# Kernel tuning notes

Hardware: AMD Instinct MI355X
Metric: run time of the kernel (lower is better)

The kernel has to match this reference:

```python
import jax, jax.numpy as jnp
import numpy as np

KH, KW = 3, 3
STRIDE, PAD, DIL = 1, 1, 1


def setup_inputs() -> dict:
    key = jax.random.key(0)
    k1, k2, k3 = jax.random.split(key, 3)
    B, C, H, W, O = 8, 128, 64, 64, 128
    x = jax.random.normal(k1, (B, C, H, W), jnp.float32)
    # offset layout: [B, 2*K, Ho, Wo], pairs (dy, dx) per kernel tap
    offset = jax.random.normal(k2, (B, 2 * KH * KW, H, W), jnp.float32)
    n = C * KH * KW
    stdv = 1.0 / np.sqrt(n)
    weight = jax.random.uniform(k3, (O, C, KH, KW), jnp.float32, -stdv, stdv)
    bias = jnp.zeros((O,), jnp.float32)
    return {"x": x, "offset": offset, "weight": weight, "bias": bias}


def _deform_conv(x, offset, weight, bias):
    B, C, H, W = x.shape
    O = weight.shape[0]
    K = KH * KW
    Ho = (H + 2 * PAD - DIL * (KH - 1) - 1) // STRIDE + 1
    Wo = (W + 2 * PAD - DIL * (KW - 1) - 1) // STRIDE + 1

    off = offset.reshape(B, K, 2, Ho, Wo)  # (dy, dx) per tap

    # base sampling grid for each kernel tap: [K, Ho, Wo]
    hs = jnp.arange(Ho, dtype=jnp.float32) * STRIDE - PAD
    ws = jnp.arange(Wo, dtype=jnp.float32) * STRIDE - PAD
    ki = jnp.arange(KH, dtype=jnp.float32) * DIL
    kj = jnp.arange(KW, dtype=jnp.float32) * DIL
    base_y = (ki[:, None, None, None] + hs[None, None, :, None])  # [KH,1,Ho,1]
    base_x = (kj[None, :, None, None] + ws[None, None, None, :])  # [1,KW,1,Wo]
    base_y = jnp.broadcast_to(base_y, (KH, KW, Ho, Wo)).reshape(K, Ho, Wo)
    base_x = jnp.broadcast_to(base_x, (KH, KW, Ho, Wo)).reshape(K, Ho, Wo)

    py = base_y[None] + off[:, :, 0]  # [B,K,Ho,Wo]
    px = base_x[None] + off[:, :, 1]

    y0 = jnp.floor(py)
    x0 = jnp.floor(px)
    ly = py - y0  # fractional parts
    lx = px - x0
    y0i = y0.astype(jnp.int32)
    x0i = x0.astype(jnp.int32)

    flat = x.reshape(B, C, H * W)

    def gather(yi, xi, w):
        # zero outside the image (DCN zero-padding semantics)
        valid = (yi >= 0) & (yi < H) & (xi >= 0) & (xi < W)
        idx = jnp.clip(yi, 0, H - 1) * W + jnp.clip(xi, 0, W - 1)  # [B,K,Ho,Wo]
        g = jnp.take_along_axis(flat, idx.reshape(B, 1, -1), axis=2)
        g = g.reshape(B, C, K, Ho, Wo)
        wmask = (w * valid.astype(x.dtype))[:, None]  # [B,1,K,Ho,Wo]
        return g * wmask

    # bilinear accumulation over 4 corners -> im2col columns [B,C,K,Ho,Wo]
    cols = gather(y0i, x0i, (1 - ly) * (1 - lx))
    cols = cols + gather(y0i, x0i + 1, (1 - ly) * lx)
    cols = cols + gather(y0i + 1, x0i, ly * (1 - lx))
    cols = cols + gather(y0i + 1, x0i + 1, ly * lx)

    out = jnp.einsum('ock,bckhw->bohw', weight.reshape(O, C, K), cols)
    return out + bias[None, :, None, None]


def reference(x, offset, weight, bias):
    return _deform_conv(x, offset, weight, bias)
```

## Files before the change

kernel.cpp:

```cpp
#include <hip/hip_runtime.h>


#define BB 8
#define CC 128
#define HH 64
#define WW 64
#define OO 128
#define KTAPS 9

typedef __attribute__((ext_vector_type(8))) short bf16x8;
typedef __attribute__((ext_vector_type(4))) float f32x4;

__device__ __forceinline__ unsigned short f2bf(float f) {
    unsigned u = __float_as_uint(f);
    u += 0x7FFFu + ((u >> 16) & 1u);
    return (unsigned short)(u >> 16);
}
#if __has_builtin(__builtin_amdgcn_cvt_pk_bf16_f32)
typedef __attribute__((ext_vector_type(2))) __bf16 bf16x2_t;
__device__ __forceinline__ unsigned pack2bf(float lo, float hi) {
    bf16x2_t v = __builtin_amdgcn_cvt_pk_bf16_f32(lo, hi);
    unsigned r;
    __builtin_memcpy(&r, &v, 4);
    return r;
}
#else
__device__ __forceinline__ unsigned pack2bf(float lo, float hi) {
    return (unsigned)f2bf(lo) | ((unsigned)f2bf(hi) << 16);
}
#endif
__device__ __forceinline__ float bflo(unsigned p) { return __uint_as_float(p << 16); }
__device__ __forceinline__ float bfhi(unsigned p) { return __uint_as_float(p & 0xFFFF0000u); }

__global__ __launch_bounds__(256)
void prep_kernel(const float* __restrict__ x, const float* __restrict__ wgt,
                 unsigned short* __restrict__ xt, unsigned short* __restrict__ wpk) {
    const int t = threadIdx.x;
    if (blockIdx.x < 512) {
        __shared__ float tile[WW * 132];
        const int b = blockIdx.x >> 6;
        const int h = blockIdx.x & 63;
        const float* src = x + ((size_t)b * CC * HH + h) * WW;
        {
            const int wq = t & 15;
            const int cb = t >> 4;
#pragma unroll
            for (int it = 0; it < 8; ++it) {
                const int c = it * 16 + cb;
                const float4 v = *reinterpret_cast<const float4*>(src + (size_t)c * (HH * WW) + wq * 4);
                tile[(wq * 4 + 0) * 132 + c] = v.x;
                tile[(wq * 4 + 1) * 132 + c] = v.y;
                tile[(wq * 4 + 2) * 132 + c] = v.z;
                tile[(wq * 4 + 3) * 132 + c] = v.w;
            }
        }
        __syncthreads();
        unsigned short* dst = xt + ((size_t)b * HH + h) * WW * CC;
        {
            const int cg = t & 15;
            const int wb = t >> 4;
#pragma unroll
            for (int it = 0; it < 4; ++it) {
                const int w = it * 16 + wb;
                const float* tp = &tile[w * 132 + cg * 8];
                uint4 p;
                p.x = pack2bf(tp[0], tp[1]);
                p.y = pack2bf(tp[2], tp[3]);
                p.z = pack2bf(tp[4], tp[5]);
                p.w = pack2bf(tp[6], tp[7]);
                *reinterpret_cast<uint4*>(&dst[(size_t)w * CC + cg * 8]) = p;
            }
        }
    } else {
        const int id   = (blockIdx.x - 512) * 256 + t;
        const int lane = id & 63;
        const int frag = id >> 6;
        const int nt   = frag & 7;
        const int c0q  = (frag >> 3) & 3;
        const int tap  = frag >> 5;
        const int o    = (nt << 4) + (lane & 15);
        const int c    = (c0q << 5) + ((lane >> 4) << 3);
        const float* s = wgt + ((size_t)o * CC + c) * KTAPS + tap;
        unsigned u[4];
#pragma unroll
        for (int j = 0; j < 4; ++j)
            u[j] = pack2bf(s[(2 * j) * KTAPS], s[(2 * j + 1) * KTAPS]);
        *reinterpret_cast<uint4*>(wpk + (size_t)frag * 512 + lane * 8) =
            make_uint4(u[0], u[1], u[2], u[3]);
    }
}

__global__ __launch_bounds__(256, 2)
void dcn_mfma_kernel(const unsigned short* __restrict__ xt,
                     const unsigned short* __restrict__ wpk,
                     const float* __restrict__ offset,
                     const float* __restrict__ bias,
                     float* __restrict__ out) {
    __shared__ __align__(16) float smem_f[4 * 128 * 20];
    float2* sLL = reinterpret_cast<float2*>(smem_f);
    short2* sYX = reinterpret_cast<short2*>(smem_f + 1152);

    const int t  = threadIdx.x;
    const int b  = blockIdx.x >> 6;
    const int ho = blockIdx.x & 63;

    for (int s = t; s < KTAPS * 64; s += 256) {
        const int k  = s >> 6;
        const int wo = s & 63;
        const int ki = k / 3;
        const int kj = k - ki * 3;
        const float dy = offset[(((size_t)b * 18 + 2 * k    ) * 64 + ho) * 64 + wo];
        const float dx = offset[(((size_t)b * 18 + 2 * k + 1) * 64 + ho) * 64 + wo];
        const float py = (float)(ho - 1 + ki) + dy;
        const float px = (float)(wo - 1 + kj) + dx;
        const float y0f = floorf(py);
        const float x0f = floorf(px);
        sLL[s] = make_float2(py - y0f, px - x0f);
        sYX[s] = make_short2((short)(int)y0f, (short)(int)x0f);
    }
    __syncthreads();

    f32x4 acc[8];
#pragma unroll
    for (int nt = 0; nt < 8; ++nt) acc[nt] = (f32x4){0.f, 0.f, 0.f, 0.f};

    const int lane = t & 63;
    const int wave = t >> 6;
    const int lm   = lane & 15;
    const int quad = lane >> 4;
    const int q16  = quad * 16;
    const int lane16 = lane * 16;
    const char* xb = (const char*)(xt + (size_t)b * HH * WW * CC);
    const char* wb = (const char*)wpk;

    for (int tap = 0; tap < KTAPS; ++tap) {
        const int rec = (tap << 6) + (wave << 4) + lm;
        const float2 ll = sLL[rec];
        const short2 yx = sYX[rec];
        const int y0 = yx.x, x0 = yx.y;
        const int y1 = y0 + 1, x1 = x0 + 1;
        const float ly = ll.x, lx = ll.y;
        const bool vy0 = ((unsigned)y0 < (unsigned)HH);
        const bool vy1 = ((unsigned)y1 < (unsigned)HH);
        const bool vx0 = ((unsigned)x0 < (unsigned)WW);
        const bool vx1 = ((unsigned)x1 < (unsigned)WW);
        const float w00 = (vy0 && vx0) ? (1.f - ly) * (1.f - lx) : 0.f;
        const float w01 = (vy0 && vx1) ? (1.f - ly) * lx         : 0.f;
        const float w10 = (vy1 && vx0) ? ly * (1.f - lx)         : 0.f;
        const float w11 = (vy1 && vx1) ? ly * lx                 : 0.f;
        const int cy0 = min(max(y0, 0), HH - 1);
        const int cy1 = min(max(y1, 0), HH - 1);
        const int cx0 = min(max(x0, 0), WW - 1);
        const int cx1 = min(max(x1, 0), WW - 1);
        const char* base00 = xb + ((((cy0 << 6) + cx0) << 8) + q16);
        const char* base01 = xb + ((((cy0 << 6) + cx1) << 8) + q16);
        const char* base10 = xb + ((((cy1 << 6) + cx0) << 8) + q16);
        const char* base11 = xb + ((((cy1 << 6) + cx1) << 8) + q16);

        uint4 a00 = *reinterpret_cast<const uint4*>(base00);
        uint4 a01 = *reinterpret_cast<const uint4*>(base01);
        uint4 a10 = *reinterpret_cast<const uint4*>(base10);
        uint4 a11 = *reinterpret_cast<const uint4*>(base11);

#pragma unroll
        for (int c0q = 0; c0q < 4; ++c0q) {
            uint4 bfr[8];
            const char* wrow = wb + ((((tap << 5) + (c0q << 3))) << 10) + lane16;
#pragma unroll
            for (int nt = 0; nt < 8; ++nt)
                bfr[nt] = *reinterpret_cast<const uint4*>(wrow + (nt << 10));
            uint4 n00, n01, n10, n11;
            if (c0q < 3) {
                const int cb = (c0q + 1) << 6;
                n00 = *reinterpret_cast<const uint4*>(base00 + cb);
                n01 = *reinterpret_cast<const uint4*>(base01 + cb);
                n10 = *reinterpret_cast<const uint4*>(base10 + cb);
                n11 = *reinterpret_cast<const uint4*>(base11 + cb);
            }
            const unsigned* u00 = reinterpret_cast<const unsigned*>(&a00);
            const unsigned* u01 = reinterpret_cast<const unsigned*>(&a01);
            const unsigned* u10 = reinterpret_cast<const unsigned*>(&a10);
            const unsigned* u11 = reinterpret_cast<const unsigned*>(&a11);
            unsigned afu[4];
#pragma unroll
            for (int j = 0; j < 4; ++j) {
                const float rl = w00 * bflo(u00[j]) + w01 * bflo(u01[j])
                               + w10 * bflo(u10[j]) + w11 * bflo(u11[j]);
                const float rh = w00 * bfhi(u00[j]) + w01 * bfhi(u01[j])
                               + w10 * bfhi(u10[j]) + w11 * bfhi(u11[j]);
                afu[j] = pack2bf(rl, rh);
            }
            bf16x8 afrag;
            __builtin_memcpy(&afrag, afu, 16);
#pragma unroll
            for (int nt = 0; nt < 8; ++nt) {
                bf16x8 bfrag;
                __builtin_memcpy(&bfrag, &bfr[nt], 16);
                acc[nt] = __builtin_amdgcn_mfma_f32_16x16x32_bf16(afrag, bfrag, acc[nt], 0, 0, 0);
            }
            if (c0q < 3) { a00 = n00; a01 = n01; a10 = n10; a11 = n11; }
        }
    }

    __syncthreads();
    float* scr = smem_f + wave * (128 * 20);
#pragma unroll
    for (int nt = 0; nt < 8; ++nt) {
        const int o_l = (nt << 4) + lm;
        *reinterpret_cast<float4*>(&scr[o_l * 20 + (quad << 2)]) =
            make_float4(acc[nt][0], acc[nt][1], acc[nt][2], acc[nt][3]);
    }
#pragma unroll
    for (int h = 0; h < 2; ++h) {
        const int o = (h << 6) + lane;
        const float bv = bias[o];
        float* op = out + (((size_t)(b * OO + o) * HH + ho) << 6) + (wave << 4);
        const float* sr = scr + o * 20;
#pragma unroll
        for (int j = 0; j < 4; ++j) {
            const float4 f = *reinterpret_cast<const float4*>(sr + j * 4);
            *reinterpret_cast<float4*>(op + j * 4) =
                make_float4(f.x + bv, f.y + bv, f.z + bv, f.w + bv);
        }
    }
}

extern "C" void kernel_launch(void* const* d_in, const int* in_sizes, int n_in,
                              void* d_out, int out_size, void* d_ws, size_t ws_size,
                              hipStream_t stream) {
    const float* x      = (const float*)d_in[0];
    const float* offset = (const float*)d_in[1];
    const float* wgt    = (const float*)d_in[2];
    const float* bias   = (const float*)d_in[3];
    float* out = (float*)d_out;

    unsigned short* xt  = (unsigned short*)d_ws;
    unsigned short* wpk = xt + (size_t)BB * HH * WW * CC;

    hipLaunchKernelGGL(prep_kernel, dim3(512 + 72), dim3(256), 0, stream, x, wgt, xt, wpk);
    hipLaunchKernelGGL(dcn_mfma_kernel, dim3(BB * HH), dim3(256), 0, stream,
                       xt, wpk, offset, bias, out);
}
```

Before: 132.6 us.

## Split output row across two blocks and split channel reduction across waves

Each block now handles half an output row (32 pixels). The four waves are arranged as two pixel groups times two channel halves, and the two channel-half partial accumulators are reduced through shared memory. The grid doubles to 1024 blocks and launch bounds rise to 4 blocks per CU, aiming at better occupancy and latency hiding on the gather-heavy loop. The cost is an extra LDS reduction step, and only half the waves do the epilogue.

```diff
diff --git a/kernel.cpp b/kernel.cpp
--- a/kernel.cpp
+++ b/kernel.cpp
@@ -90,25 +90,29 @@
     }
 }
 
-__global__ __launch_bounds__(256, 2)
+__global__ __launch_bounds__(256, 4)
 void dcn_mfma_kernel(const unsigned short* __restrict__ xt,
                      const unsigned short* __restrict__ wpk,
                      const float* __restrict__ offset,
                      const float* __restrict__ bias,
                      float* __restrict__ out) {
-    __shared__ __align__(16) float smem_f[4 * 128 * 20];
-    float2* sLL = reinterpret_cast<float2*>(smem_f);
-    short2* sYX = reinterpret_cast<short2*>(smem_f + 1152);
-
-    const int t  = threadIdx.x;
-    const int b  = blockIdx.x >> 6;
-    const int ho = blockIdx.x & 63;
-
-    for (int s = t; s < KTAPS * 64; s += 256) {
-        const int k  = s >> 6;
-        const int wo = s & 63;
-        const int ki = k / 3;
-        const int kj = k - ki * 3;
+    __shared__ __align__(16) float2 sLL[KTAPS * 32];
+    __shared__ __align__(16) short2 sYX[KTAPS * 32];
+    __shared__ __align__(16) float  dumpf[2 * 2048];
+    __shared__ __align__(16) float  transf[2 * 2560];
+
+    const int t   = threadIdx.x;
+    const int bid = blockIdx.x;
+    const int b   = bid >> 7;
+    const int ho  = (bid >> 1) & 63;
+    const int woh = bid & 1;
+
+    for (int s = t; s < KTAPS * 32; s += 256) {
+        const int k   = s >> 5;
+        const int wol = s & 31;
+        const int wo  = (woh << 5) + wol;
+        const int ki  = k / 3;
+        const int kj  = k - ki * 3;
         const float dy = offset[(((size_t)b * 18 + 2 * k    ) * 64 + ho) * 64 + wo];
         const float dx = offset[(((size_t)b * 18 + 2 * k + 1) * 64 + ho) * 64 + wo];
         const float py = (float)(ho - 1 + ki) + dy;
@@ -126,15 +130,17 @@
 
     const int lane = t & 63;
     const int wave = t >> 6;
+    const int mi   = wave & 1;
+    const int kh   = wave >> 1;
     const int lm   = lane & 15;
     const int quad = lane >> 4;
-    const int q16  = quad * 16;
-    const int lane16 = lane * 16;
     const char* xb = (const char*)(xt + (size_t)b * HH * WW * CC);
     const char* wb = (const char*)wpk;
+    const int cbase  = (kh << 7) + (quad << 4);
+    const int lane16 = lane * 16;
 
     for (int tap = 0; tap < KTAPS; ++tap) {
-        const int rec = (tap << 6) + (wave << 4) + lm;
+        const int rec = (tap << 5) + (mi << 4) + lm;
         const float2 ll = sLL[rec];
         const short2 yx = sYX[rec];
         const int y0 = yx.x, x0 = yx.y;
@@ -152,43 +158,46 @@
         const int cy1 = min(max(y1, 0), HH - 1);
         const int cx0 = min(max(x0, 0), WW - 1);
         const int cx1 = min(max(x1, 0), WW - 1);
-        const char* base00 = xb + ((((cy0 << 6) + cx0) << 8) + q16);
-        const char* base01 = xb + ((((cy0 << 6) + cx1) << 8) + q16);
-        const char* base10 = xb + ((((cy1 << 6) + cx0) << 8) + q16);
-        const char* base11 = xb + ((((cy1 << 6) + cx1) << 8) + q16);
+        const char* base00 = xb + ((((cy0 << 6) + cx0) << 8) + cbase);
+        const char* base01 = xb + ((((cy0 << 6) + cx1) << 8) + cbase);
+        const char* base10 = xb + ((((cy1 << 6) + cx0) << 8) + cbase);
+        const char* base11 = xb + ((((cy1 << 6) + cx1) << 8) + cbase);
 
         uint4 a00 = *reinterpret_cast<const uint4*>(base00);
         uint4 a01 = *reinterpret_cast<const uint4*>(base01);
         uint4 a10 = *reinterpret_cast<const uint4*>(base10);
         uint4 a11 = *reinterpret_cast<const uint4*>(base11);
-
-#pragma unroll
-        for (int c0q = 0; c0q < 4; ++c0q) {
+        uint4 c00 = *reinterpret_cast<const uint4*>(base00 + 64);
+        uint4 c01 = *reinterpret_cast<const uint4*>(base01 + 64);
+        uint4 c10 = *reinterpret_cast<const uint4*>(base10 + 64);
+        uint4 c11 = *reinterpret_cast<const uint4*>(base11 + 64);
+
+        const char* wtap = wb + ((((tap << 2) + (kh << 1)) << 13)) + lane16;
+
+#pragma unroll
+        for (int j = 0; j < 2; ++j) {
             uint4 bfr[8];
-            const char* wrow = wb + ((((tap << 5) + (c0q << 3))) << 10) + lane16;
+            const char* wrow = wtap + (j << 13);
 #pragma unroll
             for (int nt = 0; nt < 8; ++nt)
                 bfr[nt] = *reinterpret_cast<const uint4*>(wrow + (nt << 10));
-            uint4 n00, n01, n10, n11;
-            if (c0q < 3) {
-                const int cb = (c0q + 1) << 6;
-                n00 = *reinterpret_cast<const uint4*>(base00 + cb);
-                n01 = *reinterpret_cast<const uint4*>(base01 + cb);
-                n10 = *reinterpret_cast<const uint4*>(base10 + cb);
-                n11 = *reinterpret_cast<const uint4*>(base11 + cb);
-            }
-            const unsigned* u00 = reinterpret_cast<const unsigned*>(&a00);
-            const unsigned* u01 = reinterpret_cast<const unsigned*>(&a01);
-            const unsigned* u10 = reinterpret_cast<const unsigned*>(&a10);
-            const unsigned* u11 = reinterpret_cast<const unsigned*>(&a11);
+
+            const uint4 va = (j == 0) ? a00 : c00;
+            const uint4 vb = (j == 0) ? a01 : c01;
+            const uint4 vc = (j == 0) ? a10 : c10;
+            const uint4 vd = (j == 0) ? a11 : c11;
+            const unsigned* u00 = reinterpret_cast<const unsigned*>(&va);
+            const unsigned* u01 = reinterpret_cast<const unsigned*>(&vb);
+            const unsigned* u10 = reinterpret_cast<const unsigned*>(&vc);
+            const unsigned* u11 = reinterpret_cast<const unsigned*>(&vd);
             unsigned afu[4];
 #pragma unroll
-            for (int j = 0; j < 4; ++j) {
-                const float rl = w00 * bflo(u00[j]) + w01 * bflo(u01[j])
-                               + w10 * bflo(u10[j]) + w11 * bflo(u11[j]);
-                const float rh = w00 * bfhi(u00[j]) + w01 * bfhi(u01[j])
-                               + w10 * bfhi(u10[j]) + w11 * bfhi(u11[j]);
-                afu[j] = pack2bf(rl, rh);
+            for (int jj = 0; jj < 4; ++jj) {
+                const float rl = w00 * bflo(u00[jj]) + w01 * bflo(u01[jj])
+                               + w10 * bflo(u10[jj]) + w11 * bflo(u11[jj]);
+                const float rh = w00 * bfhi(u00[jj]) + w01 * bfhi(u01[jj])
+                               + w10 * bfhi(u10[jj]) + w11 * bfhi(u11[jj]);
+                afu[jj] = pack2bf(rl, rh);
             }
             bf16x8 afrag;
             __builtin_memcpy(&afrag, afu, 16);
@@ -198,29 +207,43 @@
                 __builtin_memcpy(&bfrag, &bfr[nt], 16);
                 acc[nt] = __builtin_amdgcn_mfma_f32_16x16x32_bf16(afrag, bfrag, acc[nt], 0, 0, 0);
             }
-            if (c0q < 3) { a00 = n00; a01 = n01; a10 = n10; a11 = n11; }
-        }
-    }
-
+        }
+    }
+
+    if (kh == 1) {
+        float* d = dumpf + mi * 2048;
+#pragma unroll
+        for (int nt = 0; nt < 8; ++nt)
+            *reinterpret_cast<float4*>(&d[((nt << 6) + lane) << 2]) =
+                make_float4(acc[nt][0], acc[nt][1], acc[nt][2], acc[nt][3]);
+    }
     __syncthreads();
-    float* scr = smem_f + wave * (128 * 20);
-#pragma unroll
-    for (int nt = 0; nt < 8; ++nt) {
-        const int o_l = (nt << 4) + lm;
-        *reinterpret_cast<float4*>(&scr[o_l * 20 + (quad << 2)]) =
-            make_float4(acc[nt][0], acc[nt][1], acc[nt][2], acc[nt][3]);
-    }
-#pragma unroll
-    for (int h = 0; h < 2; ++h) {
-        const int o = (h << 6) + lane;
-        const float bv = bias[o];
-        float* op = out + (((size_t)(b * OO + o) * HH + ho) << 6) + (wave << 4);
-        const float* sr = scr + o * 20;
-#pragma unroll
-        for (int j = 0; j < 4; ++j) {
-            const float4 f = *reinterpret_cast<const float4*>(sr + j * 4);
-            *reinterpret_cast<float4*>(op + j * 4) =
-                make_float4(f.x + bv, f.y + bv, f.z + bv, f.w + bv);
+    if (kh == 0) {
+        const float* d = dumpf + mi * 2048;
+#pragma unroll
+        for (int nt = 0; nt < 8; ++nt) {
+            const float4 p = *reinterpret_cast<const float4*>(&d[((nt << 6) + lane) << 2]);
+            acc[nt][0] += p.x; acc[nt][1] += p.y; acc[nt][2] += p.z; acc[nt][3] += p.w;
+        }
+        float* scr = transf + mi * 2560;
+#pragma unroll
+        for (int nt = 0; nt < 8; ++nt) {
+            const int o_l = (nt << 4) + lm;
+            *reinterpret_cast<float4*>(&scr[o_l * 20 + (quad << 2)]) =
+                make_float4(acc[nt][0], acc[nt][1], acc[nt][2], acc[nt][3]);
+        }
+#pragma unroll
+        for (int h = 0; h < 2; ++h) {
+            const int o = (h << 6) + lane;
+            const float bv = bias[o];
+            float* op = out + (((size_t)(b * OO + o) * HH + ho) << 6) + (woh << 5) + (mi << 4);
+            const float* sr = scr + o * 20;
+#pragma unroll
+            for (int jj = 0; jj < 4; ++jj) {
+                const float4 f = *reinterpret_cast<const float4*>(sr + jj * 4);
+                *reinterpret_cast<float4*>(op + jj * 4) =
+                    make_float4(f.x + bv, f.y + bv, f.z + bv, f.w + bv);
+            }
         }
     }
 }
@@ -238,6 +261,6 @@
     unsigned short* wpk = xt + (size_t)BB * HH * WW * CC;
 
     hipLaunchKernelGGL(prep_kernel, dim3(512 + 72), dim3(256), 0, stream, x, wgt, xt, wpk);
-    hipLaunchKernelGGL(dcn_mfma_kernel, dim3(BB * HH), dim3(256), 0, stream,
+    hipLaunchKernelGGL(dcn_mfma_kernel, dim3(BB * HH * 2), dim3(256), 0, stream,
                        xt, wpk, offset, bias, out);
 }
```

New measurement: 143.2 us. 1.08x slower.

## Stage per-tap weight fragments in double-buffered LDS via direct global-to-LDS loads

Applied to the files above, without the earlier changes.

Each block now copies the packed bf16 weights for one kernel tap into shared memory with global_load_lds. It double-buffers across taps so the next tap's copy overlaps the current tap's MFMA work. The B fragments are then read from LDS instead of each wave reloading them from global/L2. The block index is remapped so consecutive blocks share the same output row across batches, and the epilogue scratch stride is padded to 21 to reduce bank conflicts. This adds a __syncthreads per tap and a large LDS footprint that may limit occupancy, and float4 accesses at stride 21 are no longer 16-byte aligned.

```diff
diff --git a/kernel.cpp b/kernel.cpp
--- a/kernel.cpp
+++ b/kernel.cpp
@@ -96,17 +96,18 @@
                      const float* __restrict__ offset,
                      const float* __restrict__ bias,
                      float* __restrict__ out) {
-    __shared__ __align__(16) float smem_f[4 * 128 * 20];
-    float2* sLL = reinterpret_cast<float2*>(smem_f);
-    short2* sYX = reinterpret_cast<short2*>(smem_f + 1152);
-
-    const int t  = threadIdx.x;
-    const int b  = blockIdx.x >> 6;
-    const int ho = blockIdx.x & 63;
-
-    for (int s = t; s < KTAPS * 64; s += 256) {
-        const int k  = s >> 6;
-        const int wo = s & 63;
+    __shared__ __align__(16) unsigned short wB[2][16384];
+    __shared__ __align__(16) float2 sLL[KTAPS * 64];
+    __shared__ __align__(16) short2 sYX[KTAPS * 64];
+
+    const int t   = threadIdx.x;
+    const int bid = blockIdx.x;
+    const int b   = bid & 7;
+    const int ho  = bid >> 3;
+
+    for (int r = t; r < KTAPS * 64; r += 256) {
+        const int k  = r >> 6;
+        const int wo = r & 63;
         const int ki = k / 3;
         const int kj = k - ki * 3;
         const float dy = offset[(((size_t)b * 18 + 2 * k    ) * 64 + ho) * 64 + wo];
@@ -115,8 +116,25 @@
         const float px = (float)(wo - 1 + kj) + dx;
         const float y0f = floorf(py);
         const float x0f = floorf(px);
-        sLL[s] = make_float2(py - y0f, px - x0f);
-        sYX[s] = make_short2((short)(int)y0f, (short)(int)x0f);
+        sLL[r] = make_float2(py - y0f, px - x0f);
+        sYX[r] = make_short2((short)(int)y0f, (short)(int)x0f);
+    }
+
+    const char* wb = (const char*)wpk;
+    {
+        const char* wsrc = wb + (t << 4);
+        unsigned short* ldst = &wB[0][t << 3];
+#pragma unroll
+        for (int i = 0; i < 8; ++i) {
+#if __has_builtin(__builtin_amdgcn_global_load_lds)
+            __builtin_amdgcn_global_load_lds(
+                (const __attribute__((address_space(1))) unsigned*)(wsrc + (i << 12)),
+                (__attribute__((address_space(3))) unsigned*)(ldst + (i << 11)), 16, 0, 0);
+#else
+            *reinterpret_cast<uint4*>(ldst + (i << 11)) =
+                *reinterpret_cast<const uint4*>(wsrc + (i << 12));
+#endif
+        }
     }
     __syncthreads();
 
@@ -125,16 +143,31 @@
     for (int nt = 0; nt < 8; ++nt) acc[nt] = (f32x4){0.f, 0.f, 0.f, 0.f};
 
     const int lane = t & 63;
-    const int wave = t >> 6;
+    const int mi   = t >> 6;
     const int lm   = lane & 15;
     const int quad = lane >> 4;
-    const int q16  = quad * 16;
-    const int lane16 = lane * 16;
-    const char* xb = (const char*)(xt + (size_t)b * HH * WW * CC);
-    const char* wb = (const char*)wpk;
-
+    const char* xb = (const char*)xt + ((size_t)b << 20);
+    const int lane8 = lane << 3;
+
+    int curb = 0;
     for (int tap = 0; tap < KTAPS; ++tap) {
-        const int rec = (tap << 6) + (wave << 4) + lm;
+        if (tap < KTAPS - 1) {
+            const char* wsrc = wb + ((tap + 1) << 15) + (t << 4);
+            unsigned short* ldst = &wB[curb ^ 1][t << 3];
+#pragma unroll
+            for (int i = 0; i < 8; ++i) {
+#if __has_builtin(__builtin_amdgcn_global_load_lds)
+                __builtin_amdgcn_global_load_lds(
+                    (const __attribute__((address_space(1))) unsigned*)(wsrc + (i << 12)),
+                    (__attribute__((address_space(3))) unsigned*)(ldst + (i << 11)), 16, 0, 0);
+#else
+                *reinterpret_cast<uint4*>(ldst + (i << 11)) =
+                    *reinterpret_cast<const uint4*>(wsrc + (i << 12));
+#endif
+            }
+        }
+
+        const int rec = (tap << 6) + (mi << 4) + lm;
         const float2 ll = sLL[rec];
         const short2 yx = sYX[rec];
         const int y0 = yx.x, x0 = yx.y;
@@ -152,23 +185,26 @@
         const int cy1 = min(max(y1, 0), HH - 1);
         const int cx0 = min(max(x0, 0), WW - 1);
         const int cx1 = min(max(x1, 0), WW - 1);
-        const char* base00 = xb + ((((cy0 << 6) + cx0) << 8) + q16);
-        const char* base01 = xb + ((((cy0 << 6) + cx1) << 8) + q16);
-        const char* base10 = xb + ((((cy1 << 6) + cx0) << 8) + q16);
-        const char* base11 = xb + ((((cy1 << 6) + cx1) << 8) + q16);
+        const char* base00 = xb + ((((cy0 << 6) + cx0) << 8) + (quad << 4));
+        const char* base01 = xb + ((((cy0 << 6) + cx1) << 8) + (quad << 4));
+        const char* base10 = xb + ((((cy1 << 6) + cx0) << 8) + (quad << 4));
+        const char* base11 = xb + ((((cy1 << 6) + cx1) << 8) + (quad << 4));
 
         uint4 a00 = *reinterpret_cast<const uint4*>(base00);
         uint4 a01 = *reinterpret_cast<const uint4*>(base01);
         uint4 a10 = *reinterpret_cast<const uint4*>(base10);
         uint4 a11 = *reinterpret_cast<const uint4*>(base11);
 
+        const unsigned short* bbuf = wB[curb];
+
 #pragma unroll
         for (int c0q = 0; c0q < 4; ++c0q) {
-            uint4 bfr[8];
-            const char* wrow = wb + ((((tap << 5) + (c0q << 3))) << 10) + lane16;
+            bf16x8 bfr[8];
 #pragma unroll
             for (int nt = 0; nt < 8; ++nt)
-                bfr[nt] = *reinterpret_cast<const uint4*>(wrow + (nt << 10));
+                bfr[nt] = *reinterpret_cast<const bf16x8*>(
+                    bbuf + (((c0q << 3) + nt) << 9) + lane8);
+
             uint4 n00, n01, n10, n11;
             if (c0q < 3) {
                 const int cb = (c0q + 1) << 6;
@@ -177,49 +213,48 @@
                 n10 = *reinterpret_cast<const uint4*>(base10 + cb);
                 n11 = *reinterpret_cast<const uint4*>(base11 + cb);
             }
+
             const unsigned* u00 = reinterpret_cast<const unsigned*>(&a00);
             const unsigned* u01 = reinterpret_cast<const unsigned*>(&a01);
             const unsigned* u10 = reinterpret_cast<const unsigned*>(&a10);
             const unsigned* u11 = reinterpret_cast<const unsigned*>(&a11);
             unsigned afu[4];
 #pragma unroll
-            for (int j = 0; j < 4; ++j) {
-                const float rl = w00 * bflo(u00[j]) + w01 * bflo(u01[j])
-                               + w10 * bflo(u10[j]) + w11 * bflo(u11[j]);
-                const float rh = w00 * bfhi(u00[j]) + w01 * bfhi(u01[j])
-                               + w10 * bfhi(u10[j]) + w11 * bfhi(u11[j]);
-                afu[j] = pack2bf(rl, rh);
+            for (int jj = 0; jj < 4; ++jj) {
+                const float rl = w00 * bflo(u00[jj]) + w01 * bflo(u01[jj])
+                               + w10 * bflo(u10[jj]) + w11 * bflo(u11[jj]);
+                const float rh = w00 * bfhi(u00[jj]) + w01 * bfhi(u01[jj])
+                               + w10 * bfhi(u10[jj]) + w11 * bfhi(u11[jj]);
+                afu[jj] = pack2bf(rl, rh);
             }
             bf16x8 afrag;
             __builtin_memcpy(&afrag, afu, 16);
 #pragma unroll
-            for (int nt = 0; nt < 8; ++nt) {
-                bf16x8 bfrag;
-                __builtin_memcpy(&bfrag, &bfr[nt], 16);
-                acc[nt] = __builtin_amdgcn_mfma_f32_16x16x32_bf16(afrag, bfrag, acc[nt], 0, 0, 0);
-            }
+            for (int nt = 0; nt < 8; ++nt)
+                acc[nt] = __builtin_amdgcn_mfma_f32_16x16x32_bf16(afrag, bfr[nt], acc[nt], 0, 0, 0);
             if (c0q < 3) { a00 = n00; a01 = n01; a10 = n10; a11 = n11; }
         }
-    }
-
-    __syncthreads();
-    float* scr = smem_f + wave * (128 * 20);
+        __syncthreads();
+        curb ^= 1;
+    }
+
+    float* scr = reinterpret_cast<float*>(&wB[0][0]) + mi * 2688;
 #pragma unroll
     for (int nt = 0; nt < 8; ++nt) {
         const int o_l = (nt << 4) + lm;
-        *reinterpret_cast<float4*>(&scr[o_l * 20 + (quad << 2)]) =
+        *reinterpret_cast<float4*>(&scr[o_l * 21 + (quad << 2)]) =
             make_float4(acc[nt][0], acc[nt][1], acc[nt][2], acc[nt][3]);
     }
 #pragma unroll
     for (int h = 0; h < 2; ++h) {
         const int o = (h << 6) + lane;
         const float bv = bias[o];
-        float* op = out + (((size_t)(b * OO + o) * HH + ho) << 6) + (wave << 4);
-        const float* sr = scr + o * 20;
-#pragma unroll
-        for (int j = 0; j < 4; ++j) {
-            const float4 f = *reinterpret_cast<const float4*>(sr + j * 4);
-            *reinterpret_cast<float4*>(op + j * 4) =
+        float* op = out + (((size_t)(b * OO + o) * HH + ho) << 6) + (mi << 4);
+        const float* sr = scr + o * 21;
+#pragma unroll
+        for (int jj = 0; jj < 4; ++jj) {
+            const float4 f = *reinterpret_cast<const float4*>(sr + jj * 4);
+            *reinterpret_cast<float4*>(op + jj * 4) =
                 make_float4(f.x + bv, f.y + bv, f.z + bv, f.w + bv);
         }
     }
@@ -238,6 +273,6 @@
     unsigned short* wpk = xt + (size_t)BB * HH * WW * CC;
 
     hipLaunchKernelGGL(prep_kernel, dim3(512 + 72), dim3(256), 0, stream, x, wgt, xt, wpk);
-    hipLaunchKernelGGL(dcn_mfma_kernel, dim3(BB * HH), dim3(256), 0, stream,
+    hipLaunchKernelGGL(dcn_mfma_kernel, dim3(512), dim3(256), 0, stream,
                        xt, wpk, offset, bias, out);
 }
```

Measured after the change: 136.2 us. 1.03x slower.
